# Kernel optimization log

Measured on AMD Instinct MI355X. Metric: run time of the kernel, lower is better.

## Reference

```python
import jax, jax.numpy as jnp
import numpy as np

MC = 16384
N_STEPS = 120
PERIOD = 30
N_MAT = 4
N_STR = 21
WIDTH_DIFF = 50
WIDTH_VAN = 30
WIDTH_EXO = 20
N_HIDDEN = 3  # n_layers=4 -> input layer + 3 hidden layers + output layer
R = 0.05
TIMEGRID = jnp.asarray(np.linspace(0.0, 1.0, N_STEPS + 1).astype(np.float32))
STRIKES = jnp.asarray(np.linspace(0.8, 1.2, N_STR).astype(np.float32))


def _init_net(key, d_in, width, d_out):
    ks = jax.random.split(key, 6)
    f = lambda k, shape, fan: jax.random.normal(k, shape, jnp.float32) / np.sqrt(fan).astype(np.float32)
    return dict(
        W0=f(ks[0], (N_MAT, d_in, width), d_in),
        b0=f(ks[1], (N_MAT, width), width),
        hW=f(ks[2], (N_MAT, N_HIDDEN, width, width), width),
        hb=f(ks[3], (N_MAT, N_HIDDEN, width), width),
        Wo=f(ks[4], (N_MAT, width, d_out), width),
        bo=f(ks[5], (N_MAT, d_out), width),
    )


def setup_inputs() -> dict:
    key = jax.random.key(0)
    kz, kd, kv, ke = jax.random.split(key, 4)
    inp = {
        "S0": jnp.ones((1,), jnp.float32),
        "z": jax.random.normal(kz, (MC, N_STEPS), jnp.float32),
    }
    for name, net in (("d", _init_net(kd, 2, WIDTH_DIFF, 1)),
                      ("v", _init_net(kv, 2, WIDTH_VAN, N_STR * N_MAT)),
                      ("e", _init_net(ke, N_STEPS + 2, WIDTH_EXO, 1))):
        for pn, arr in net.items():
            inp[name + pn] = arr
    inp["MC_samples"] = MC
    inp["ind_T"] = N_STEPS
    inp["period_length"] = PERIOD
    return inp


def _mlp(x, W0, b0, hW, hb, Wo, bo, softplus_out):
    h = jax.nn.relu(x @ W0 + b0)
    for k in range(hW.shape[0]):  # static small number of hidden layers
        h = jax.nn.relu(h @ hW[k] + hb[k])
    y = h @ Wo + bo
    return jax.nn.softplus(y) if softplus_out else y


def _forward(S0, z, dW0, db0, dhW, dhb, dWo, dbo,
             vW0, vb0, vhW, vhb, vWo, vbo,
             eW0, eb0, ehW, ehb, eWo, ebo,
             MC_samples, ind_T, period_length, remat=False):
    sg = jax.lax.stop_gradient
    S_init = jnp.ones((MC_samples, 1), jnp.float32) * S0
    path0 = jnp.zeros((MC_samples, N_STEPS + 1), jnp.float32).at[:, 0].set(S_init[:, 0])
    zeros_mat = jnp.zeros((N_MAT, N_STR), jnp.float32)

    def step(carry, i):
        S_old, cv_v, cv_e, run_max, path, pv, pvv = carry
        idx = (i - 1) // period_length
        t0 = TIMEGRID[i - 1]
        h = TIMEGRID[i] - TIMEGRID[i - 1]
        sqh = jnp.sqrt(h)
        dWn = sqh * jax.lax.dynamic_slice_in_dim(z, i - 1, 1, 1)  # (MC,1)
        t = jnp.full_like(S_old, t0)
        diff = _mlp(jnp.concatenate([t, S_old], 1),
                    dW0[idx], db0[idx], dhW[idx], dhb[idx], dWo[idx], dbo[idx], True)
        Sd, diffd = sg(S_old), sg(diff)
        S_new = (S_old
                 + R * S_old * h / (1.0 + R * Sd * sqh)
                 + S_old * diff * dWn / (1.0 + Sd * diffd * sqh))
        disc = jnp.exp(-R * t0)
        cv_v = cv_v + disc * Sd * diffd * dWn * _mlp(
            jnp.concatenate([t, Sd], 1),
            vW0[idx], vb0[idx], vhW[idx], vhb[idx], vWo[idx], vbo[idx], False)
        cv_e = cv_e + disc * Sd * diffd * dWn * _mlp(
            jnp.concatenate([t, path], 1),
            eW0[idx], eb0[idx], ehW[idx], ehb[idx], eWo[idx], ebo[idx], False)
        path = jax.lax.dynamic_update_slice(path, sg(S_new), (0, i))
        run_max = jnp.maximum(run_max, S_new)
        # vanilla prices at maturities (i multiple of period_length)
        ind_m = i // period_length - 1
        disc_i = jnp.exp(-R * TIMEGRID[i])
        cv_row = jax.lax.dynamic_slice_in_dim(
            cv_v.reshape(MC_samples, N_MAT, N_STR), ind_m, 1, 1)[:, 0, :]
        pr = disc_i * jnp.maximum(S_new - STRIKES[None, :], 0.0) - cv_row  # (MC, N_STR)
        is_mat = (i % period_length) == 0
        pv = jnp.where(is_mat, jax.lax.dynamic_update_index_in_dim(pv, pr.mean(0), ind_m, 0), pv)
        pvv = jnp.where(is_mat, jax.lax.dynamic_update_index_in_dim(pvv, jnp.var(pr, axis=0, ddof=1), ind_m, 0), pvv)
        return (S_new, cv_v, cv_e, run_max, path, pv, pvv), None

    body = jax.checkpoint(step) if remat else step
    carry0 = (S_init,
              jnp.zeros((MC_samples, N_STR * N_MAT), jnp.float32),
              jnp.zeros((MC_samples, 1), jnp.float32),
              S_init, path0, zeros_mat, zeros_mat)
    (S_T, cv_v, cv_e, run_max, path, pv, pvv), _ = jax.lax.scan(
        body, carry0, jnp.arange(1, ind_T + 1))

    sgv = jax.lax.stop_gradient
    exotic = run_max - S_T
    discT = jnp.exp(-R * TIMEGRID[ind_T])
    e = discT * exotic
    error = sgv(e) - jnp.mean(sgv(e)) - sgv(cv_e)
    price_exo = e - cv_e
    return pv, pvv, price_exo, price_exo.mean(), jnp.var(price_exo, ddof=1), error


def reference(S0, z, dW0, db0, dhW, dhb, dWo, dbo,
              vW0, vb0, vhW, vhb, vWo, vbo,
              eW0, eb0, ehW, ehb, eWo, ebo,
              MC_samples, ind_T, period_length):
    return _forward(S0, z, dW0, db0, dhW, dhb, dWo, dbo,
                    vW0, vb0, vhW, vhb, vWo, vbo,
                    eW0, eb0, ehW, ehb, eWo, ebo,
                    MC_samples, ind_T, period_length)
```

## Files before the change

### kernel.cpp

```cpp
#include <hip/hip_runtime.h>
#include <hip/hip_bf16.h>
#include <math.h>

#define MC      16384
#define NSTEPS  120
#define PER     30
#define NMAT    4
#define NSTR    21
#define RRATE   0.05f
#define NBLK    512
#define NSAMP   32
#define HSTEP   (1.0f/120.0f)
#define SQH     0.09128709291752769f

typedef short short8  __attribute__((ext_vector_type(8)));
typedef short short4v __attribute__((ext_vector_type(4)));
typedef float f32x4   __attribute__((ext_vector_type(4)));

#define WS_PRPART 0
#define WS_EPART  (NMAT*NSTR*2*NBLK)
#define WS_MEANE  (WS_EPART + NBLK)
#define WS_FRAGS  86784

#define OUT_PV    0
#define OUT_PVV   84
#define OUT_PEXO  168
#define OUT_MEAN  16552
#define OUT_VAR   16553
#define OUT_ERR   16554

__device__ __forceinline__ float tgridf(int i)  { return (float)i * HSTEP; }
__device__ __forceinline__ float strikef(int s) { return (float)(0.8 + (double)s * 0.02); }
__device__ __forceinline__ float softplusf(float x){
  return fmaxf(x, 0.0f) + __logf(1.0f + __expf(-fabsf(x)));
}
__device__ __forceinline__ unsigned short f2bf(float f){
  __hip_bfloat16 b = __float2bfloat16(f);
  return __builtin_bit_cast(unsigned short, b);
}
__device__ __forceinline__ float bf2f(unsigned short u){
  return __builtin_bit_cast(float, ((unsigned)u)<<16);
}
__device__ __forceinline__ int swaddr(int row, int slot, int inner){
  return row*256 + (((slot + row) & 15) << 4) + inner;
}
__device__ __forceinline__ short8 rdA(const unsigned short* H, int mt, int base, int lane){
  int addr = swaddr(mt*16 + (lane&15), base + (lane>>4), 0);
  return *(const short8*)((const char*)H + addr);
}
__device__ __forceinline__ f32x4 mm(short8 a, short8 b, f32x4 c){
  return __builtin_amdgcn_mfma_f32_16x16x32_bf16(a, b, c, 0, 0, 0);
}
__device__ __forceinline__ void stD(unsigned short* H, int colbase, int mt, int lane,
                                    f32x4 acc, bool relu){
  int col  = colbase + (lane & 15);
  int slot = col >> 3, inner = (col & 7)*2;
  #pragma unroll
  for (int i2=0;i2<4;++i2){
    int rw = mt*16 + ((lane>>4)<<2) + i2;
    float v = acc[i2];
    if (relu) v = fmaxf(v, 0.0f);
    *(unsigned short*)((char*)H + swaddr(rw, slot, inner)) = f2bf(v);
  }
}
__device__ __forceinline__ short8 mkBd(const float* __restrict__ W, const float* __restrict__ bias,
                                       int n0, int kt, int lane){
  short8 r;
  int n = n0 + (lane&15);
  #pragma unroll
  for (int i2=0;i2<8;++i2){
    int k = kt*32 + ((lane>>4)<<3) + i2;
    float w;
    if (k<50)       w = (n<50)? W[k*50+n] : 0.f;
    else if (k==50) w = (n<50)? bias[n] : ((n==50)? 1.f : 0.f);
    else            w = 0.f;
    r[i2] = (short)f2bf(w);
  }
  return r;
}
__device__ __forceinline__ short8 mkBq(const float* __restrict__ W, const float* __restrict__ bias,
                                       int KV, int n0, int lane){
  short8 r;
  int n = n0 + (lane&15);
  #pragma unroll
  for (int i2=0;i2<8;++i2){
    int k = ((lane>>4)<<3) + i2;
    float w;
    if (k<KV)       w = (n<KV)? W[k*KV+n] : 0.f;
    else if (k==KV) w = (n<KV)? bias[n] : ((n==KV)? 1.f : 0.f);
    else            w = 0.f;
    r[i2] = (short)f2bf(w);
  }
  return r;
}

extern "C" __global__ void mk_frags(
    const float* __restrict__ dhW, const float* __restrict__ dhb,
    const float* __restrict__ vhW, const float* __restrict__ vhb,
    const float* __restrict__ ehW, const float* __restrict__ ehb,
    float* __restrict__ ws)
{
  const int bid = blockIdx.x;
  const int p   = bid / 36;
  const int fid = bid % 36;
  const int lane = threadIdx.x;
  short8 fr;
  if (fid < 24){
    int l = fid >> 3, nt = (fid >> 1) & 3, kt = fid & 1;
    fr = mkBd(dhW + p*7500 + l*2500, dhb + p*150 + l*50, nt*16, kt, lane);
  } else if (fid < 30){
    int q = fid - 24, l = q >> 1, nt = q & 1;
    fr = mkBq(vhW + p*2700 + l*900, vhb + p*90 + l*30, 30, nt*16, lane);
  } else {
    int q = fid - 30, l = q >> 1, nt = q & 1;
    fr = mkBq(ehW + p*1200 + l*400, ehb + p*60 + l*20, 20, nt*16, lane);
  }
  ((short8*)(ws + WS_FRAGS))[(p*36 + fid)*64 + lane] = fr;
}

extern "C" __global__ void __launch_bounds__(256,3) mc_main(
    const float* __restrict__ S0p, const float* __restrict__ z,
    const float* __restrict__ dW0, const float* __restrict__ db0,
    const float* __restrict__ dhW, const float* __restrict__ dhb,
    const float* __restrict__ dWo, const float* __restrict__ dbo,
    const float* __restrict__ vW0, const float* __restrict__ vb0,
    const float* __restrict__ vhW, const float* __restrict__ vhb,
    const float* __restrict__ vWo, const float* __restrict__ vbo,
    const float* __restrict__ eW0, const float* __restrict__ eb0,
    const float* __restrict__ ehW, const float* __restrict__ ehb,
    const float* __restrict__ eWo, const float* __restrict__ ebo,
    float* __restrict__ out, float* __restrict__ ws)
{
  __shared__ unsigned short Hb0[NSAMP*128];
  __shared__ unsigned short Hb1[NSAMP*128];
  __shared__ float vh3f[NSAMP*40];
  __shared__ float zper[NSAMP*30];
  __shared__ float eW0per[NMAT*600];
  __shared__ float dW0s[128];
  __shared__ float db0s[64];
  __shared__ float vW0s[64];
  __shared__ float vb0s[32];
  __shared__ float eW0ts[20];
  __shared__ float eb0s[20];
  __shared__ float dWoL[64];
  __shared__ float eWoL[32];
  __shared__ float dtab[PER];
  __shared__ float Sb[NSAMP], ebuf[NSAMP];
  __shared__ float part[2*84*2];

  const int tid  = threadIdx.x;
  const int lane = tid & 63;
  const int wid  = __builtin_amdgcn_readfirstlane(tid >> 6);
  const int blk  = blockIdx.x;
  const int r    = tid >> 3;
  const int cc   = tid & 7;

  const bool isv = (wid < 2);
  const int  ntd = wid;
  const int  ntq = wid & 1;

  const float S0v = S0p[0];
  float S = S0v, runmax = S0v, cvE = 0.f;
  f32x4 rr[3];
  #pragma unroll
  for (int q=0;q<3;++q){ rr[q][0]=0.f; rr[q][1]=0.f; rr[q][2]=0.f; rr[q][3]=0.f; }
  float aE[NMAT][4];
  #pragma unroll
  for (int mt2=0;mt2<NMAT;++mt2){ aE[mt2][0]=0.f; aE[mt2][1]=0.f; aE[mt2][2]=0.f; aE[mt2][3]=0.f; }
  float G_[4] = {0.f,0.f,0.f,0.f};

  #pragma unroll 1
  for (int p=0;p<NMAT;++p){
    for (int q=tid; q<NSAMP*30; q+=256){ int r2=q/30, c2=q%30; zper[q] = z[(size_t)(blk*NSAMP+r2)*NSTEPS + p*30 + c2]; }
    for (int q=tid; q<NMAT*600; q+=256){ int mat=q/600, k=q%600; eW0per[q] = eW0[mat*2440 + p*600 + 20 + k]; }
    if (tid < 128){
      int rw = tid>>6, j = tid&63;
      dW0s[tid] = (j<50)? dW0[p*100 + rw*50 + j] : 0.f;
    } else if (tid < 192){
      int j = tid-128;
      db0s[j] = (j<50)? db0[p*50+j] : ((j==50)? 1.f : 0.f);
    } else {
      int idx = tid-192, rw = idx>>5, j = idx&31;
      vW0s[idx] = (j<30)? vW0[p*60 + rw*30 + j] : 0.f;
    }
    if (tid < 32)       vb0s[tid] = (tid<30)? vb0[p*30+tid] : ((tid==30)? 1.f : 0.f);
    else if (tid < 52){ int j=tid-32; eW0ts[j]=eW0[p*2440+j]; eb0s[j]=eb0[p*20+j]; }
    else if (tid < 116){ int j=tid-52; dWoL[j] = (j<50)? dWo[p*50+j] : 0.f; }
    else if (tid < 148){ int j=tid-116; eWoL[j] = (j<20)? eWo[p*20+j] : 0.f; }
    else if (tid < 148+PER){ int j=tid-148; dtab[j] = __expf(-RRATE * ((float)(p*PER+j) * HSTEP)); }

    const float dboS = dbo[p], eboS = ebo[p];
    const int fqB = (isv? 24 : 30) + ntq;

    __syncthreads();

    #pragma unroll 1
    for (int ii=1; ii<=PER; ++ii){
      const float t0  = tgridf(p*PER + ii - 1);

      const short8* FB;
      { uintptr_t u = (uintptr_t)(ws + WS_FRAGS); asm volatile("" : "+s"(u)); FB = (const short8*)u; }
      const short8* FBp = FB + (size_t)p*36*64 + lane;

      {
        short8 hv;
        #pragma unroll
        for (int k=0;k<8;++k){
          int j = cc*8 + k;
          float u = fmaxf(fmaf(t0, dW0s[j], fmaf(S, dW0s[64+j], db0s[j])), 0.f);
          hv[k] = (short)f2bf(u);
        }
        *(short8*)((char*)Hb0 + swaddr(r, cc, 0)) = hv;
        short4v vv;
        #pragma unroll
        for (int k=0;k<4;++k){
          int j = cc*4 + k;
          float u = fmaxf(fmaf(t0, vW0s[j], fmaf(S, vW0s[32+j], vb0s[j])), 0.f);
          vv[k] = (short)f2bf(u);
        }
        *(short4v*)((char*)Hb0 + swaddr(r, 8+(cc>>1), (cc&1)*8)) = vv;
        short4v ev = {0,0,0,0};
        if (cc < 5){
          const int o = (ii-1)*20 + cc*4;
          f32x4 w0 = *(const f32x4*)&eW0per[        o];
          f32x4 w1 = *(const f32x4*)&eW0per[ 600 +  o];
          f32x4 w2 = *(const f32x4*)&eW0per[1200 +  o];
          f32x4 w3 = *(const f32x4*)&eW0per[1800 +  o];
          #pragma unroll
          for (int k=0;k<4;++k){
            aE[0][k] = fmaf(S, w0[k], aE[0][k]);
            aE[1][k] = fmaf(S, w1[k], aE[1][k]);
            aE[2][k] = fmaf(S, w2[k], aE[2][k]);
            aE[3][k] = fmaf(S, w3[k], aE[3][k]);
            float a = (p==0)?aE[0][k]:(p==1)?aE[1][k]:(p==2)?aE[2][k]:aE[3][k];
            int j = cc*4 + k;
            float e0 = fmaxf(t0*eW0ts[j] + a + eb0s[j], 0.f);
            ev[k] = (short)f2bf(e0);
          }
        } else if (cc == 5){
          ev[0] = (short)0x3F80;
        }
        *(short4v*)((char*)Hb0 + swaddr(r, 12+(cc>>1), (cc&1)*8)) = ev;
      }
      __syncthreads();
      {
        short8 b0 = FBp[(0 + ntd*2 + 0)*64], b1 = FBp[(0 + ntd*2 + 1)*64];
        short8 Bq = FBp[fqB*64];
        short8 a00=rdA(Hb0,0,0,lane), a01=rdA(Hb0,0,4,lane);
        short8 a10=rdA(Hb0,1,0,lane), a11=rdA(Hb0,1,4,lane);
        f32x4 c0={0.f,0.f,0.f,0.f}, c1={0.f,0.f,0.f,0.f};
        c0=mm(a00,b0,c0); c0=mm(a01,b1,c0);
        c1=mm(a10,b0,c1); c1=mm(a11,b1,c1);
        stD(Hb1, ntd*16, 0, lane, c0, true);
        stD(Hb1, ntd*16, 1, lane, c1, true);
        short8 q0=rdA(Hb0,0,isv?8:12,lane), q1=rdA(Hb0,1,isv?8:12,lane);
        f32x4 cq0={0.f,0.f,0.f,0.f}, cq1={0.f,0.f,0.f,0.f};
        cq0=mm(q0,Bq,cq0); cq1=mm(q1,Bq,cq1);
        stD(Hb1, (isv?64:96)+ntq*16, 0, lane, cq0, true);
        stD(Hb1, (isv?64:96)+ntq*16, 1, lane, cq1, true);
      }
      __syncthreads();
      {
        short8 b0 = FBp[(8 + ntd*2 + 0)*64], b1 = FBp[(8 + ntd*2 + 1)*64];
        short8 Bq = FBp[(fqB+2)*64];
        short8 a00=rdA(Hb1,0,0,lane), a01=rdA(Hb1,0,4,lane);
        short8 a10=rdA(Hb1,1,0,lane), a11=rdA(Hb1,1,4,lane);
        f32x4 c0={0.f,0.f,0.f,0.f}, c1={0.f,0.f,0.f,0.f};
        c0=mm(a00,b0,c0); c0=mm(a01,b1,c0);
        c1=mm(a10,b0,c1); c1=mm(a11,b1,c1);
        stD(Hb0, ntd*16, 0, lane, c0, true);
        stD(Hb0, ntd*16, 1, lane, c1, true);
        short8 q0=rdA(Hb1,0,isv?8:12,lane), q1=rdA(Hb1,1,isv?8:12,lane);
        f32x4 cq0={0.f,0.f,0.f,0.f}, cq1={0.f,0.f,0.f,0.f};
        cq0=mm(q0,Bq,cq0); cq1=mm(q1,Bq,cq1);
        stD(Hb0, (isv?64:96)+ntq*16, 0, lane, cq0, true);
        stD(Hb0, (isv?64:96)+ntq*16, 1, lane, cq1, true);
      }
      __syncthreads();
      {
        short8 b0 = FBp[(16 + ntd*2 + 0)*64], b1 = FBp[(16 + ntd*2 + 1)*64];
        short8 Bq = FBp[(fqB+4)*64];
        short8 a00=rdA(Hb0,0,0,lane), a01=rdA(Hb0,0,4,lane);
        short8 a10=rdA(Hb0,1,0,lane), a11=rdA(Hb0,1,4,lane);
        f32x4 c0={0.f,0.f,0.f,0.f}, c1={0.f,0.f,0.f,0.f};
        c0=mm(a00,b0,c0); c0=mm(a01,b1,c0);
        c1=mm(a10,b0,c1); c1=mm(a11,b1,c1);
        stD(Hb1, ntd*16, 0, lane, c0, true);
        stD(Hb1, ntd*16, 1, lane, c1, true);
        short8 q0=rdA(Hb0,0,isv?8:12,lane), q1=rdA(Hb0,1,isv?8:12,lane);
        f32x4 cq0={0.f,0.f,0.f,0.f}, cq1={0.f,0.f,0.f,0.f};
        cq0=mm(q0,Bq,cq0); cq1=mm(q1,Bq,cq1);
        if (isv){
          #pragma unroll
          for (int i2=0;i2<4;++i2){
            int r0 = ((lane>>4)<<2) + i2;
            vh3f[ r0     *40 + ntq*16 + (lane&15)] = fmaxf(cq0[i2], 0.f);
            vh3f[(16+r0) *40 + ntq*16 + (lane&15)] = fmaxf(cq1[i2], 0.f);
          }
        } else {
          stD(Hb1, 96+ntq*16, 0, lane, cq0, true);
          stD(Hb1, 96+ntq*16, 1, lane, cq1, true);
        }
      }
      __syncthreads();
      {
        float yp = 0.f;
        {
          short8 hv = *(const short8*)((const char*)Hb1 + swaddr(r, cc, 0));
          #pragma unroll
          for (int k=0;k<8;++k) yp = fmaf(bf2f((unsigned short)hv[k]), dWoL[cc*8+k], yp);
        }
        float yep = 0.f;
        if (cc < 5){
          short4v hv = *(const short4v*)((const char*)Hb1 + swaddr(r, 12+(cc>>1), (cc&1)*8));
          #pragma unroll
          for (int k=0;k<4;++k) yep = fmaf(bf2f((unsigned short)hv[k]), eWoL[cc*4+k], yep);
        }
        #pragma unroll
        for (int mk=1; mk<8; mk<<=1){ yp += __shfl_xor(yp, mk); yep += __shfl_xor(yep, mk); }
        const float y    = yp + dboS;
        const float diff = softplusf(y);
        const float zv   = zper[r*30 + (ii-1)];
        const float dWn  = SQH * zv;
        const float d1 = 1.f + (RRATE*SQH)*S;
        const float d2 = 1.f + S*diff*SQH;
        const float Snew = S + (RRATE*HSTEP)*S*__builtin_amdgcn_rcpf(d1)
                             + S*diff*dWn*__builtin_amdgcn_rcpf(d2);
        const float disc = dtab[ii-1];
        const float coef = disc * S * diff * dWn;
        cvE = fmaf(coef, yep + eboS, cvE);
        runmax = fmaxf(runmax, Snew);
        {
          f32x4 vv = *(const f32x4*)&vh3f[r*40 + cc*4];
          #pragma unroll
          for (int k=0;k<4;++k) G_[k] = fmaf(coef, vv[k], G_[k]);
        }
        S = Snew;

        if (ii==PER){
          short4v gv;
          #pragma unroll
          for (int k=0;k<4;++k){ gv[k] = (short)f2bf(G_[k]); G_[k] = 0.f; }
          *(short4v*)((char*)Hb0 + swaddr(r, cc>>1, (cc&1)*8)) = gv;
          if (cc==0) Sb[r] = S;
        }
      }

      if (ii==PER){
        __syncthreads();
        const float disc_i = __expf(-RRATE * ((float)(p+1) * 0.25f));
        const float* vWop = vWo + p*2520;
        const float* vbop = vbo + p*84;
        #pragma unroll
        for (int q3=0;q3<3;++q3){
          const int T = wid*3 + q3;
          const int mtr = T/6, ntr = T%6;
          short8 a = rdA(Hb0, mtr, 0, lane);
          const int col = ntr*16 + (lane&15);
          short8 bw;
          #pragma unroll
          for (int i2=0;i2<8;++i2){
            int k = ((lane>>4)<<3)+i2;
            float w = 0.f;
            if (col < 84){
              if (k < 30)       w = vWop[k*84+col];
              else if (k == 30) w = vbop[col];
            }
            bw[i2] = (short)f2bf(w);
          }
          f32x4 d4 = {0.f,0.f,0.f,0.f};
          d4 = mm(a,bw,d4);
          const int s = col - p*NSTR;
          const bool inr = (s>=0) && (s<NSTR) && (col<84);
          const float K = strikef(s);
          float ssum=0.f, ssq=0.f;
          #pragma unroll
          for (int i2=0;i2<4;++i2){
            int row = mtr*16 + ((lane>>4)<<2) + i2;
            rr[q3][i2] += d4[i2];
            if (inr){
              float pr = disc_i*fmaxf(Sb[row]-K,0.f) - rr[q3][i2];
              ssum += pr; ssq = fmaf(pr,pr,ssq);
            }
          }
          ssum += __shfl_down(ssum,16); ssum += __shfl_down(ssum,32);
          ssq  += __shfl_down(ssq ,16); ssq  += __shfl_down(ssq ,32);
          if (inr && lane<16){
            part[(mtr*84+col)*2+0] = ssum;
            part[(mtr*84+col)*2+1] = ssq;
          }
        }
        __syncthreads();
        if (tid < NSTR){
          int cidx = p*NSTR + tid;
          ws[WS_PRPART + (cidx*2+0)*NBLK + blk] = part[cidx*2] + part[(84+cidx)*2];
        } else if (tid >= 64 && tid < 64+NSTR){
          int cidx = p*NSTR + (tid-64);
          ws[WS_PRPART + (cidx*2+1)*NBLK + blk] = part[cidx*2+1] + part[(84+cidx)*2+1];
        }
        __syncthreads();
      }
    }
  }

  if (cc==0){
    const float discT = __expf(-RRATE);
    const float e = discT * (runmax - S);
    out[OUT_PEXO + blk*NSAMP + r] = e - cvE;
    ebuf[r] = e;
  }
  __syncthreads();
  if (tid < 32){
    float se = ebuf[tid];
    se += __shfl_down(se,16); se += __shfl_down(se,8);
    se += __shfl_down(se,4);  se += __shfl_down(se,2); se += __shfl_down(se,1);
    if (tid==0) ws[WS_EPART + blk] = se;
  }
}

extern "C" __global__ void fin_pv(const float* __restrict__ ws, float* __restrict__ out){
  const int t = threadIdx.x;
  if (t >= NMAT*NSTR) return;
  float sum=0.0f, ssq=0.0f;
  for (int b=0;b<NBLK;++b){
    sum += ws[WS_PRPART + (t*2+0)*NBLK + b];
    ssq += ws[WS_PRPART + (t*2+1)*NBLK + b];
  }
  out[OUT_PV  + t] = sum * (1.0f/MC);
  out[OUT_PVV + t] = (ssq - sum*sum*(1.0f/MC)) * (1.0f/(MC-1));
}

extern "C" __global__ void fin_pe(float* out, float* ws){
  __shared__ float sA[4], sB[4], sC[4];
  const int t = threadIdx.x;
  float sum=0.0f, ssq=0.0f;
  for (int idx=t; idx<MC; idx+=256){
    const float v = out[OUT_PEXO+idx];
    sum += v; ssq = fmaf(v,v,ssq);
  }
  float es = ws[WS_EPART + t] + ws[WS_EPART + 256 + t];
  for (int o=32;o>0;o>>=1){
    sum += __shfl_down(sum,o);
    ssq += __shfl_down(ssq,o);
    es  += __shfl_down(es,o);
  }
  const int w=t>>6, lane=t&63;
  if (lane==0){ sA[w]=sum; sB[w]=ssq; sC[w]=es; }
  __syncthreads();
  if (t==0){
    const float s=sA[0]+sA[1]+sA[2]+sA[3];
    const float q=sB[0]+sB[1]+sB[2]+sB[3];
    const float e=sC[0]+sC[1]+sC[2]+sC[3];
    out[OUT_MEAN]=s*(1.0f/MC);
    out[OUT_VAR]=(q - s*s*(1.0f/MC))*(1.0f/(MC-1));
    ws[WS_MEANE]=e*(1.0f/MC);
  }
}

extern "C" __global__ void fin_err(float* out, const float* __restrict__ ws){
  const int m = blockIdx.x*blockDim.x + threadIdx.x;
  if (m < MC) out[OUT_ERR+m] = out[OUT_PEXO+m] - ws[WS_MEANE];
}

extern "C" void kernel_launch(void* const* d_in, const int* in_sizes, int n_in,
                              void* d_out, int out_size, void* d_ws, size_t ws_size,
                              hipStream_t stream){
  (void)in_sizes; (void)n_in; (void)out_size; (void)ws_size;
  const float* S0 =(const float*)d_in[0];
  const float* z  =(const float*)d_in[1];
  const float* dW0=(const float*)d_in[2];
  const float* db0=(const float*)d_in[3];
  const float* dhW=(const float*)d_in[4];
  const float* dhb=(const float*)d_in[5];
  const float* dWo=(const float*)d_in[6];
  const float* dbo=(const float*)d_in[7];
  const float* vW0=(const float*)d_in[8];
  const float* vb0=(const float*)d_in[9];
  const float* vhW=(const float*)d_in[10];
  const float* vhb=(const float*)d_in[11];
  const float* vWo=(const float*)d_in[12];
  const float* vbo=(const float*)d_in[13];
  const float* eW0=(const float*)d_in[14];
  const float* eb0=(const float*)d_in[15];
  const float* ehW=(const float*)d_in[16];
  const float* ehb=(const float*)d_in[17];
  const float* eWo=(const float*)d_in[18];
  const float* ebo=(const float*)d_in[19];
  float* out=(float*)d_out;
  float* ws =(float*)d_ws;

  mk_frags<<<dim3(NMAT*36),dim3(64),0,stream>>>(dhW,dhb,vhW,vhb,ehW,ehb,ws);
  mc_main<<<dim3(NBLK),dim3(256),0,stream>>>(S0,z,dW0,db0,dhW,dhb,dWo,dbo,
                                             vW0,vb0,vhW,vhb,vWo,vbo,
                                             eW0,eb0,ehW,ehb,eWo,ebo,out,ws);
  fin_pv <<<dim3(1), dim3(128),0,stream>>>(ws,out);
  fin_pe <<<dim3(1), dim3(256),0,stream>>>(out,ws);
  fin_err<<<dim3(64),dim3(256),0,stream>>>(out,ws);
}
```

Measured before the change: 492.3 us.

## Halve samples per block and double block count with two-wave blocks

Measured after the change: 447.6 us. 1.1x faster.

```diff
diff --git a/kernel.cpp b/kernel.cpp
--- a/kernel.cpp
+++ b/kernel.cpp
@@ -8,8 +8,8 @@
 #define NMAT    4
 #define NSTR    21
 #define RRATE   0.05f
-#define NBLK    512
-#define NSAMP   32
+#define NBLK    1024
+#define NSAMP   16
 #define HSTEP   (1.0f/120.0f)
 #define SQH     0.09128709291752769f
 
@@ -20,7 +20,7 @@
 #define WS_PRPART 0
 #define WS_EPART  (NMAT*NSTR*2*NBLK)
 #define WS_MEANE  (WS_EPART + NBLK)
-#define WS_FRAGS  86784
+#define WS_FRAGS  (WS_MEANE + 3)
 
 #define OUT_PV    0
 #define OUT_PVV   84
@@ -44,20 +44,20 @@
 __device__ __forceinline__ int swaddr(int row, int slot, int inner){
   return row*256 + (((slot + row) & 15) << 4) + inner;
 }
-__device__ __forceinline__ short8 rdA(const unsigned short* H, int mt, int base, int lane){
-  int addr = swaddr(mt*16 + (lane&15), base + (lane>>4), 0);
+__device__ __forceinline__ short8 rdA(const unsigned short* H, int base, int lane){
+  int addr = swaddr(lane&15, base + (lane>>4), 0);
   return *(const short8*)((const char*)H + addr);
 }
 __device__ __forceinline__ f32x4 mm(short8 a, short8 b, f32x4 c){
   return __builtin_amdgcn_mfma_f32_16x16x32_bf16(a, b, c, 0, 0, 0);
 }
-__device__ __forceinline__ void stD(unsigned short* H, int colbase, int mt, int lane,
+__device__ __forceinline__ void stD(unsigned short* H, int colbase, int lane,
                                     f32x4 acc, bool relu){
   int col  = colbase + (lane & 15);
   int slot = col >> 3, inner = (col & 7)*2;
   #pragma unroll
   for (int i2=0;i2<4;++i2){
-    int rw = mt*16 + ((lane>>4)<<2) + i2;
+    int rw = ((lane>>4)<<2) + i2;
     float v = acc[i2];
     if (relu) v = fmaxf(v, 0.0f);
     *(unsigned short*)((char*)H + swaddr(rw, slot, inner)) = f2bf(v);
@@ -118,7 +118,7 @@
   ((short8*)(ws + WS_FRAGS))[(p*36 + fid)*64 + lane] = fr;
 }
 
-extern "C" __global__ void __launch_bounds__(256,3) mc_main(
+extern "C" __global__ void __launch_bounds__(128,2) mc_main(
     const float* __restrict__ S0p, const float* __restrict__ z,
     const float* __restrict__ dW0, const float* __restrict__ db0,
     const float* __restrict__ dhW, const float* __restrict__ dhb,
@@ -146,7 +146,7 @@
   __shared__ float eWoL[32];
   __shared__ float dtab[PER];
   __shared__ float Sb[NSAMP], ebuf[NSAMP];
-  __shared__ float part[2*84*2];
+  __shared__ float part[84*2];
 
   const int tid  = threadIdx.x;
   const int lane = tid & 63;
@@ -155,9 +155,8 @@
   const int r    = tid >> 3;
   const int cc   = tid & 7;
 
-  const bool isv = (wid < 2);
-  const int  ntd = wid;
-  const int  ntq = wid & 1;
+  const bool isv = (wid == 0);
+  const int  ntA = wid*2, ntB = wid*2+1;
 
   const float S0v = S0p[0];
   float S = S0v, runmax = S0v, cvE = 0.f;
@@ -171,26 +170,19 @@
 
   #pragma unroll 1
   for (int p=0;p<NMAT;++p){
-    for (int q=tid; q<NSAMP*30; q+=256){ int r2=q/30, c2=q%30; zper[q] = z[(size_t)(blk*NSAMP+r2)*NSTEPS + p*30 + c2]; }
-    for (int q=tid; q<NMAT*600; q+=256){ int mat=q/600, k=q%600; eW0per[q] = eW0[mat*2440 + p*600 + 20 + k]; }
-    if (tid < 128){
-      int rw = tid>>6, j = tid&63;
-      dW0s[tid] = (j<50)? dW0[p*100 + rw*50 + j] : 0.f;
-    } else if (tid < 192){
-      int j = tid-128;
-      db0s[j] = (j<50)? db0[p*50+j] : ((j==50)? 1.f : 0.f);
-    } else {
-      int idx = tid-192, rw = idx>>5, j = idx&31;
-      vW0s[idx] = (j<30)? vW0[p*60 + rw*30 + j] : 0.f;
-    }
+    for (int q=tid; q<NSAMP*30; q+=128){ int r2=q/30, c2=q%30; zper[q] = z[(size_t)(blk*NSAMP+r2)*NSTEPS + p*30 + c2]; }
+    for (int q=tid; q<NMAT*600; q+=128){ int mat=q/600, k=q%600; eW0per[q] = eW0[mat*2440 + p*600 + 20 + k]; }
+    { int rw = tid>>6, j = tid&63; dW0s[tid] = (j<50)? dW0[p*100 + rw*50 + j] : 0.f; }
+    if (tid < 64) db0s[tid] = (tid<50)? db0[p*50+tid] : ((tid==50)? 1.f : 0.f);
+    else { int idx = tid-64, rw = idx>>5, j = idx&31; vW0s[idx] = (j<30)? vW0[p*60 + rw*30 + j] : 0.f; }
     if (tid < 32)       vb0s[tid] = (tid<30)? vb0[p*30+tid] : ((tid==30)? 1.f : 0.f);
-    else if (tid < 52){ int j=tid-32; eW0ts[j]=eW0[p*2440+j]; eb0s[j]=eb0[p*20+j]; }
-    else if (tid < 116){ int j=tid-52; dWoL[j] = (j<50)? dWo[p*50+j] : 0.f; }
-    else if (tid < 148){ int j=tid-116; eWoL[j] = (j<20)? eWo[p*20+j] : 0.f; }
-    else if (tid < 148+PER){ int j=tid-148; dtab[j] = __expf(-RRATE * ((float)(p*PER+j) * HSTEP)); }
+    else if (tid < 64){ int j=tid-32; if (j<20){ eW0ts[j]=eW0[p*2440+j]; eb0s[j]=eb0[p*20+j]; } }
+    else { int j=tid-64; dWoL[j] = (j<50)? dWo[p*50+j] : 0.f; }
+    if (tid < 32)       eWoL[tid] = (tid<20)? eWo[p*20+tid] : 0.f;
+    else if (tid < 62){ int j=tid-32; dtab[j] = __expf(-RRATE * ((float)(p*PER+j) * HSTEP)); }
 
     const float dboS = dbo[p], eboS = ebo[p];
-    const int fqB = (isv? 24 : 30) + ntq;
+    const int fq0 = isv ? 24 : 30;
 
     __syncthreads();
 
@@ -198,9 +190,9 @@
     for (int ii=1; ii<=PER; ++ii){
       const float t0  = tgridf(p*PER + ii - 1);
 
-      const short8* FB;
-      { uintptr_t u = (uintptr_t)(ws + WS_FRAGS); asm volatile("" : "+s"(u)); FB = (const short8*)u; }
-      const short8* FBp = FB + (size_t)p*36*64 + lane;
+      const short8* FBp;
+      { uintptr_t u = (uintptr_t)(ws + WS_FRAGS); asm volatile("" : "+s"(u));
+        FBp = (const short8*)u + (size_t)p*36*64 + lane; }
 
       {
         short8 hv;
@@ -244,62 +236,62 @@
       }
       __syncthreads();
       {
-        short8 b0 = FBp[(0 + ntd*2 + 0)*64], b1 = FBp[(0 + ntd*2 + 1)*64];
-        short8 Bq = FBp[fqB*64];
-        short8 a00=rdA(Hb0,0,0,lane), a01=rdA(Hb0,0,4,lane);
-        short8 a10=rdA(Hb0,1,0,lane), a11=rdA(Hb0,1,4,lane);
+        short8 bA0 = FBp[(ntA*2+0)*64], bA1 = FBp[(ntA*2+1)*64];
+        short8 bB0 = FBp[(ntB*2+0)*64], bB1 = FBp[(ntB*2+1)*64];
+        short8 Bq0 = FBp[(fq0+0)*64],   Bq1 = FBp[(fq0+1)*64];
+        short8 a0 = rdA(Hb0,0,lane), a1 = rdA(Hb0,4,lane);
+        short8 aq = rdA(Hb0, isv?8:12, lane);
         f32x4 c0={0.f,0.f,0.f,0.f}, c1={0.f,0.f,0.f,0.f};
-        c0=mm(a00,b0,c0); c0=mm(a01,b1,c0);
-        c1=mm(a10,b0,c1); c1=mm(a11,b1,c1);
-        stD(Hb1, ntd*16, 0, lane, c0, true);
-        stD(Hb1, ntd*16, 1, lane, c1, true);
-        short8 q0=rdA(Hb0,0,isv?8:12,lane), q1=rdA(Hb0,1,isv?8:12,lane);
+        c0=mm(a0,bA0,c0); c0=mm(a1,bA1,c0);
+        c1=mm(a0,bB0,c1); c1=mm(a1,bB1,c1);
+        stD(Hb1, ntA*16, lane, c0, true);
+        stD(Hb1, ntB*16, lane, c1, true);
         f32x4 cq0={0.f,0.f,0.f,0.f}, cq1={0.f,0.f,0.f,0.f};
-        cq0=mm(q0,Bq,cq0); cq1=mm(q1,Bq,cq1);
-        stD(Hb1, (isv?64:96)+ntq*16, 0, lane, cq0, true);
-        stD(Hb1, (isv?64:96)+ntq*16, 1, lane, cq1, true);
+        cq0=mm(aq,Bq0,cq0); cq1=mm(aq,Bq1,cq1);
+        stD(Hb1, (isv?64:96)+0,  lane, cq0, true);
+        stD(Hb1, (isv?64:96)+16, lane, cq1, true);
       }
       __syncthreads();
       {
-        short8 b0 = FBp[(8 + ntd*2 + 0)*64], b1 = FBp[(8 + ntd*2 + 1)*64];
-        short8 Bq = FBp[(fqB+2)*64];
-        short8 a00=rdA(Hb1,0,0,lane), a01=rdA(Hb1,0,4,lane);
-        short8 a10=rdA(Hb1,1,0,lane), a11=rdA(Hb1,1,4,lane);
+        short8 bA0 = FBp[(8+ntA*2+0)*64], bA1 = FBp[(8+ntA*2+1)*64];
+        short8 bB0 = FBp[(8+ntB*2+0)*64], bB1 = FBp[(8+ntB*2+1)*64];
+        short8 Bq0 = FBp[(fq0+2+0)*64],   Bq1 = FBp[(fq0+2+1)*64];
+        short8 a0 = rdA(Hb1,0,lane), a1 = rdA(Hb1,4,lane);
+        short8 aq = rdA(Hb1, isv?8:12, lane);
         f32x4 c0={0.f,0.f,0.f,0.f}, c1={0.f,0.f,0.f,0.f};
-        c0=mm(a00,b0,c0); c0=mm(a01,b1,c0);
-        c1=mm(a10,b0,c1); c1=mm(a11,b1,c1);
-        stD(Hb0, ntd*16, 0, lane, c0, true);
-        stD(Hb0, ntd*16, 1, lane, c1, true);
-        short8 q0=rdA(Hb1,0,isv?8:12,lane), q1=rdA(Hb1,1,isv?8:12,lane);
+        c0=mm(a0,bA0,c0); c0=mm(a1,bA1,c0);
+        c1=mm(a0,bB0,c1); c1=mm(a1,bB1,c1);
+        stD(Hb0, ntA*16, lane, c0, true);
+        stD(Hb0, ntB*16, lane, c1, true);
         f32x4 cq0={0.f,0.f,0.f,0.f}, cq1={0.f,0.f,0.f,0.f};
-        cq0=mm(q0,Bq,cq0); cq1=mm(q1,Bq,cq1);
-        stD(Hb0, (isv?64:96)+ntq*16, 0, lane, cq0, true);
-        stD(Hb0, (isv?64:96)+ntq*16, 1, lane, cq1, true);
+        cq0=mm(aq,Bq0,cq0); cq1=mm(aq,Bq1,cq1);
+        stD(Hb0, (isv?64:96)+0,  lane, cq0, true);
+        stD(Hb0, (isv?64:96)+16, lane, cq1, true);
       }
       __syncthreads();
       {
-        short8 b0 = FBp[(16 + ntd*2 + 0)*64], b1 = FBp[(16 + ntd*2 + 1)*64];
-        short8 Bq = FBp[(fqB+4)*64];
-        short8 a00=rdA(Hb0,0,0,lane), a01=rdA(Hb0,0,4,lane);
-        short8 a10=rdA(Hb0,1,0,lane), a11=rdA(Hb0,1,4,lane);
+        short8 bA0 = FBp[(16+ntA*2+0)*64], bA1 = FBp[(16+ntA*2+1)*64];
+        short8 bB0 = FBp[(16+ntB*2+0)*64], bB1 = FBp[(16+ntB*2+1)*64];
+        short8 Bq0 = FBp[(fq0+4+0)*64],    Bq1 = FBp[(fq0+4+1)*64];
+        short8 a0 = rdA(Hb0,0,lane), a1 = rdA(Hb0,4,lane);
+        short8 aq = rdA(Hb0, isv?8:12, lane);
         f32x4 c0={0.f,0.f,0.f,0.f}, c1={0.f,0.f,0.f,0.f};
-        c0=mm(a00,b0,c0); c0=mm(a01,b1,c0);
-        c1=mm(a10,b0,c1); c1=mm(a11,b1,c1);
-        stD(Hb1, ntd*16, 0, lane, c0, true);
-        stD(Hb1, ntd*16, 1, lane, c1, true);
-        short8 q0=rdA(Hb0,0,isv?8:12,lane), q1=rdA(Hb0,1,isv?8:12,lane);
+        c0=mm(a0,bA0,c0); c0=mm(a1,bA1,c0);
+        c1=mm(a0,bB0,c1); c1=mm(a1,bB1,c1);
+        stD(Hb1, ntA*16, lane, c0, true);
+        stD(Hb1, ntB*16, lane, c1, true);
         f32x4 cq0={0.f,0.f,0.f,0.f}, cq1={0.f,0.f,0.f,0.f};
-        cq0=mm(q0,Bq,cq0); cq1=mm(q1,Bq,cq1);
+        cq0=mm(aq,Bq0,cq0); cq1=mm(aq,Bq1,cq1);
         if (isv){
           #pragma unroll
           for (int i2=0;i2<4;++i2){
             int r0 = ((lane>>4)<<2) + i2;
-            vh3f[ r0     *40 + ntq*16 + (lane&15)] = fmaxf(cq0[i2], 0.f);
-            vh3f[(16+r0) *40 + ntq*16 + (lane&15)] = fmaxf(cq1[i2], 0.f);
+            vh3f[r0*40 +      (lane&15)] = fmaxf(cq0[i2], 0.f);
+            vh3f[r0*40 + 16 + (lane&15)] = fmaxf(cq1[i2], 0.f);
           }
         } else {
-          stD(Hb1, 96+ntq*16, 0, lane, cq0, true);
-          stD(Hb1, 96+ntq*16, 1, lane, cq1, true);
+          stD(Hb1, 96+0,  lane, cq0, true);
+          stD(Hb1, 96+16, lane, cq1, true);
         }
       }
       __syncthreads();
@@ -353,9 +345,8 @@
         const float* vbop = vbo + p*84;
         #pragma unroll
         for (int q3=0;q3<3;++q3){
-          const int T = wid*3 + q3;
-          const int mtr = T/6, ntr = T%6;
-          short8 a = rdA(Hb0, mtr, 0, lane);
+          const int ntr = wid*3 + q3;
+          short8 a = rdA(Hb0, 0, lane);
           const int col = ntr*16 + (lane&15);
           short8 bw;
           #pragma unroll
@@ -376,7 +367,7 @@
           float ssum=0.f, ssq=0.f;
           #pragma unroll
           for (int i2=0;i2<4;++i2){
-            int row = mtr*16 + ((lane>>4)<<2) + i2;
+            int row = ((lane>>4)<<2) + i2;
             rr[q3][i2] += d4[i2];
             if (inr){
               float pr = disc_i*fmaxf(Sb[row]-K,0.f) - rr[q3][i2];
@@ -386,17 +377,17 @@
           ssum += __shfl_down(ssum,16); ssum += __shfl_down(ssum,32);
           ssq  += __shfl_down(ssq ,16); ssq  += __shfl_down(ssq ,32);
           if (inr && lane<16){
-            part[(mtr*84+col)*2+0] = ssum;
-            part[(mtr*84+col)*2+1] = ssq;
+            part[col*2+0] = ssum;
+            part[col*2+1] = ssq;
           }
         }
         __syncthreads();
         if (tid < NSTR){
           int cidx = p*NSTR + tid;
-          ws[WS_PRPART + (cidx*2+0)*NBLK + blk] = part[cidx*2] + part[(84+cidx)*2];
+          ws[WS_PRPART + (cidx*2+0)*NBLK + blk] = part[cidx*2];
         } else if (tid >= 64 && tid < 64+NSTR){
           int cidx = p*NSTR + (tid-64);
-          ws[WS_PRPART + (cidx*2+1)*NBLK + blk] = part[cidx*2+1] + part[(84+cidx)*2+1];
+          ws[WS_PRPART + (cidx*2+1)*NBLK + blk] = part[cidx*2+1];
         }
         __syncthreads();
       }
@@ -410,10 +401,10 @@
     ebuf[r] = e;
   }
   __syncthreads();
-  if (tid < 32){
+  if (tid < 16){
     float se = ebuf[tid];
-    se += __shfl_down(se,16); se += __shfl_down(se,8);
-    se += __shfl_down(se,4);  se += __shfl_down(se,2); se += __shfl_down(se,1);
+    se += __shfl_down(se,8); se += __shfl_down(se,4);
+    se += __shfl_down(se,2); se += __shfl_down(se,1);
     if (tid==0) ws[WS_EPART + blk] = se;
   }
 }
@@ -438,7 +429,8 @@
     const float v = out[OUT_PEXO+idx];
     sum += v; ssq = fmaf(v,v,ssq);
   }
-  float es = ws[WS_EPART + t] + ws[WS_EPART + 256 + t];
+  float es = 0.0f;
+  for (int idx=t; idx<NBLK; idx+=256) es += ws[WS_EPART + idx];
   for (int o=32;o>0;o>>=1){
     sum += __shfl_down(sum,o);
     ssq += __shfl_down(ssq,o);
@@ -490,7 +482,7 @@
   float* ws =(float*)d_ws;
 
   mk_frags<<<dim3(NMAT*36),dim3(64),0,stream>>>(dhW,dhb,vhW,vhb,ehW,ehb,ws);
-  mc_main<<<dim3(NBLK),dim3(256),0,stream>>>(S0,z,dW0,db0,dhW,dhb,dWo,dbo,
+  mc_main<<<dim3(NBLK),dim3(128),0,stream>>>(S0,z,dW0,db0,dhW,dhb,dWo,dbo,
                                              vW0,vb0,vhW,vhb,vWo,vbo,
                                              eW0,eb0,ehW,ehb,eWo,ebo,out,ws);
   fin_pv <<<dim3(1), dim3(128),0,stream>>>(ws,out);
```
